# Performance work log

Measured on AMD Instinct MI355X. Metric: run time of the kernel, lower is better.

## Reference

```python
import jax, jax.numpy as jnp
import numpy as np

NODE_FEAT = 200  # F.interpolate size in run_all_node
TOPN = 2         # StitchModel.topn


def _node_feats(img, mask, flow, n_inst, max_pix):
    """Vectorized run_all_node: per-instance gather, linear interp to NODE_FEAT,
    3x3 sign histogram of flow[:2], mean of flow[2]. mask holds labels 1..n_inst;
    max_pix is a static upper bound on pixels per instance."""
    flat = mask.reshape(-1) - 1                       # labels 0..N-1
    order = jnp.argsort(flat)                         # stable sort by label
    counts = jax.ops.segment_sum(jnp.ones_like(flat), flat, num_segments=n_inst)
    starts = jnp.concatenate([jnp.zeros((1,), counts.dtype), jnp.cumsum(counts)[:-1]])
    j = jnp.arange(max_pix)
    pos = starts[:, None] + jnp.minimum(j[None, :], counts[:, None] - 1)
    idx = order[pos]                                  # [N, max_pix] padded pixel indices
    valid = j[None, :] < counts[:, None]              # [N, max_pix]
    iv = img.reshape(-1)[idx]                         # instance intensity profiles
    fx = flow[0].reshape(-1)[idx]
    fy = flow[1].reshape(-1)[idx]
    fz = flow[2].reshape(-1)[idx]
    cf = counts.astype(img.dtype)
    zflow = jnp.where(valid, fz, 0).sum(1) / cf       # flows[-1][m].mean()

    def interp(v, L):                                 # torch linear interp, align_corners=False
        Lf = L.astype(img.dtype)
        p = jnp.clip((jnp.arange(NODE_FEAT, dtype=img.dtype) + 0.5) * (Lf / NODE_FEAT) - 0.5,
                     0.0, Lf - 1.0)
        i0 = jnp.floor(p).astype(jnp.int32)
        i1 = jnp.minimum(i0 + 1, L - 1)
        w = p - i0.astype(img.dtype)
        return v[i0] * (1 - w) + v[i1] * w

    nodes = jax.vmap(interp)(iv, counts)              # [N, 200]
    # hist_flow_vector: bins ordered (x:<0,==0,>0) x (y:<0,==0,>0) -> 3*cx+cy
    cx = jnp.where(fx < 0, 0, jnp.where(fx == 0, 1, 2))
    cy = jnp.where(fy < 0, 0, jnp.where(fy == 0, 1, 2))
    bins = cx * 3 + cy
    oh = (bins[..., None] == jnp.arange(9)) & valid[..., None]
    hist = oh.sum(1).astype(img.dtype)                # [N, 9]
    return jnp.concatenate([nodes, hist], -1), zflow


def setup_inputs() -> dict:
    H = W = 2048
    N = 4096
    pix = (H * W) // N
    key = jax.random.key(0)
    ks = jax.random.split(key, 8)

    def make_mask(k):
        labels = (jnp.arange(H * W, dtype=jnp.int32) // pix) + 1   # labels 1..N
        perm = jax.random.permutation(k, H * W)
        return labels[perm].reshape(H, W)

    def make_bbox(k):
        u = jax.random.uniform(k, (N, 4), jnp.float32)
        centers = u[:, :2] * H
        sizes = u[:, 2:] * 49.0 + 1.0                               # nonzero w/h (asserted)
        return jnp.concatenate([centers, sizes], -1)

    return {
        "img1": jax.random.normal(ks[0], (H, W), jnp.float32),
        "img2": jax.random.normal(ks[1], (H, W), jnp.float32),
        "flow1": jax.random.normal(ks[2], (3, H, W), jnp.float32),
        "flow2": jax.random.normal(ks[3], (3, H, W), jnp.float32),
        "bbox1": make_bbox(ks[4]),
        "bbox2": make_bbox(ks[5]),
        "mask1": make_mask(ks[6]),
        "mask2": make_mask(ks[7]),
    }


def reference(img1, img2, flow1, flow2, bbox1, bbox2, mask1, mask2):
    N1, N2 = bbox1.shape[0], bbox2.shape[0]
    max1 = mask1.size // N1   # static bound on pixels/instance (equal-partition masks)
    max2 = mask2.size // N2
    node1, zf1 = _node_feats(img1, mask1, flow1, N1, max1)
    node2, zf2 = _node_feats(img2, mask2, flow2, N2, max2)
    x = jnp.concatenate([node1, node2], 0)            # [(N1+N2), 209]
    # build_one_graph_low_ram: per row, TOPN smallest center distances
    d = jnp.sqrt(((bbox1[:, None, :2] - bbox2[None, :, :2]) ** 2).sum(-1))  # [N1,N2]
    _, nbr = jax.lax.top_k(-d, TOPN)                  # smallest-first, like argsort[:topn]
    src = jnp.repeat(jnp.arange(N1), TOPN)            # [N1*TOPN]
    dst = nbr.reshape(-1)
    edge_index = jnp.stack([src, dst + N1])           # [2, N1*TOPN]
    edge_attr = jnp.stack([
        zf1[src], zf2[dst],
        bbox1[src, 0] - bbox2[dst, 0],
        bbox1[src, 1] - bbox2[dst, 1],
        bbox1[src, 2] / bbox2[dst, 2],
        bbox1[src, 3] / bbox2[dst, 3],
    ], -1)                                            # [N1*TOPN, 6]
    return x, edge_index, edge_attr
```

## Files before the change

### kernel.cpp

```cpp
#include <hip/hip_runtime.h>
#include <math.h>

#pragma clang fp contract(off)

#define HW      (2048*2048)
#define NI      4096
#define MAXPIX  1024
#define NF      200
#define FEAT    209
#define NE      (NI*2)
#define XSIZE   ((2*NI)*FEAT)
#define EIOFF   XSIZE
#define EAOFF   (EIOFF + 2*NE)

#define S       4096
#define CHK     (HW/S)
#define TOTCHK  (2*CHK)
#define NBPI    256
#define LPB     16
#define NBG     (2*NBPI)
#define REC     (2*HW)
#define CBLK    (TOTCHK/4)
#define BTOT    (LPB*MAXPIX)

template<int NB>
__device__ __forceinline__ unsigned long long match_bits(int v) {
    unsigned long long m = ~0ull;
    #pragma unroll
    for (int bit = 0; bit < NB; ++bit) {
        unsigned long long bb = __ballot((v >> bit) & 1);
        m &= ((v >> bit) & 1) ? bb : ~bb;
    }
    return m;
}

__global__ void __launch_bounds__(256) count_zf_kernel(const int* __restrict__ mask1,
        const int* __restrict__ mask2, const float* __restrict__ flow1,
        const float* __restrict__ flow2, unsigned* __restrict__ cntA,
        float* __restrict__ zfpart) {
    __shared__ unsigned cnt[4][NBPI];
    __shared__ float zfp[NI];
    int w = threadIdx.x >> 6, lane = threadIdx.x & 63;
    for (int j = threadIdx.x; j < 4*NBPI; j += 256) ((unsigned*)cnt)[j] = 0u;
    for (int j = threadIdx.x; j < NI; j += 256) zfp[j] = 0.f;
    __syncthreads();
    int c = blockIdx.x * 4 + w;
    int img = c / CHK;
    const int4*   mask  = (const int4*)(img ? mask2 : mask1);
    const float4* flowz = (const float4*)((img ? flow2 : flow1) + 2L*HW);
    long base4 = (long)(c - img*CHK) * (S/4);
    for (int t = 0; t < S/4; t += 64) {
        int4   l4 = mask[base4 + t + lane];
        float4 fz = flowz[base4 + t + lane];
        atomicAdd(&cnt[w][(l4.x-1) >> 4], 1u);
        atomicAdd(&cnt[w][(l4.y-1) >> 4], 1u);
        atomicAdd(&cnt[w][(l4.z-1) >> 4], 1u);
        atomicAdd(&cnt[w][(l4.w-1) >> 4], 1u);
        atomicAdd(&zfp[l4.x-1], fz.x);
        atomicAdd(&zfp[l4.y-1], fz.y);
        atomicAdd(&zfp[l4.z-1], fz.z);
        atomicAdd(&zfp[l4.w-1], fz.w);
    }
    __syncthreads();
    unsigned* dst = cntA + (long)c * NBPI;
    for (int j = lane; j < NBPI; j += 64) dst[j] = cnt[w][j];
    float* zdst = zfpart + (long)blockIdx.x * NI;
    for (int j = threadIdx.x; j < NI; j += 256) zdst[j] = zfp[j];
}

__global__ void __launch_bounds__(256) scan1_zf_kernel(unsigned* __restrict__ cntA,
        const float* __restrict__ zfpart, float* __restrict__ zfm) {
    __shared__ int wsum[4];
    __shared__ float zsh[4][LPB];
    int gb = blockIdx.x;
    int img = gb >> 8, lb = gb & (NBPI - 1);
    int t = threadIdx.x, lane = t & 63, w = t >> 6;
    const int PER = CHK / 256;
    unsigned e[PER]; int s = 0;
    long base = ((long)img * CHK + (long)t * PER) * NBPI + lb;
    #pragma unroll
    for (int i = 0; i < PER; ++i) { e[i] = cntA[base + (long)i * NBPI]; s += (int)e[i]; }
    int incl = s;
    #pragma unroll
    for (int off = 1; off < 64; off <<= 1) {
        int o = __shfl_up(incl, off);
        if (lane >= off) incl += o;
    }
    if (lane == 63) wsum[w] = incl;
    __syncthreads();
    int add = 0;
    for (int q = 0; q < w; ++q) add += wsum[q];
    unsigned pre = (unsigned)(incl + add - s);
    #pragma unroll
    for (int i = 0; i < PER; ++i) { unsigned cv = e[i]; cntA[base + (long)i * NBPI] = pre; pre += cv; }
    {
        int li0 = gb * LPB;
        int zimg = li0 >> 12, l0 = li0 & (NI-1);
        const float4* zp = (const float4*)(zfpart + (long)zimg*(CBLK/2)*NI + (long)t*NI + l0);
        float4 a0 = zp[0], a1 = zp[1], a2 = zp[2], a3 = zp[3];
        #pragma unroll
        for (int off = 1; off < 64; off <<= 1) {
            a0.x += __shfl_xor(a0.x, off); a0.y += __shfl_xor(a0.y, off);
            a0.z += __shfl_xor(a0.z, off); a0.w += __shfl_xor(a0.w, off);
            a1.x += __shfl_xor(a1.x, off); a1.y += __shfl_xor(a1.y, off);
            a1.z += __shfl_xor(a1.z, off); a1.w += __shfl_xor(a1.w, off);
            a2.x += __shfl_xor(a2.x, off); a2.y += __shfl_xor(a2.y, off);
            a2.z += __shfl_xor(a2.z, off); a2.w += __shfl_xor(a2.w, off);
            a3.x += __shfl_xor(a3.x, off); a3.y += __shfl_xor(a3.y, off);
            a3.z += __shfl_xor(a3.z, off); a3.w += __shfl_xor(a3.w, off);
        }
        if (lane == 0) {
            zsh[w][0]=a0.x; zsh[w][1]=a0.y; zsh[w][2]=a0.z; zsh[w][3]=a0.w;
            zsh[w][4]=a1.x; zsh[w][5]=a1.y; zsh[w][6]=a1.z; zsh[w][7]=a1.w;
            zsh[w][8]=a2.x; zsh[w][9]=a2.y; zsh[w][10]=a2.z; zsh[w][11]=a2.w;
            zsh[w][12]=a3.x; zsh[w][13]=a3.y; zsh[w][14]=a3.z; zsh[w][15]=a3.w;
        }
        __syncthreads();
        if (t < LPB) {
            float sum = zsh[0][t] + zsh[1][t] + zsh[2][t] + zsh[3][t];
            zfm[gb*LPB + t] = sum * (1.0f/(float)MAXPIX);
        }
    }
}

__global__ void __launch_bounds__(512) sort_kernel(
        const float* __restrict__ img1, const float* __restrict__ img2,
        const float* __restrict__ flow1, const float* __restrict__ flow2,
        const int* __restrict__ mask1, const int* __restrict__ mask2,
        const unsigned* __restrict__ cntA,
        float* __restrict__ riv, unsigned char* __restrict__ rmeta) {
    __shared__ float ivs[S];
    __shared__ unsigned short smeta[S];
    __shared__ unsigned short cw[8][NBPI];
    __shared__ int gofs[NBPI];
    __shared__ int wsum[4];
    int t = threadIdx.x, w = t >> 6, lane = t & 63;
    int c = blockIdx.x;
    int img = c / CHK;
    const int*   mask  = img ? mask2  : mask1;
    const float* image = img ? img2   : img1;
    const float* flow  = img ? flow2  : flow1;
    long base = (long)(c - img*CHK) * S;
    for (int j = t; j < 8*NBPI; j += 512) ((unsigned short*)cw)[j] = 0;
    __syncthreads();
    long qbase = base + (long)w * (S/8);
    int   pk[8];
    float piv[8];
    unsigned long long ltmask = (1ull << lane) - 1ull;
    #pragma unroll
    for (int it = 0; it < 8; ++it) {
        long p = qbase + it*64 + lane;
        int l = mask[p] - 1;
        piv[it] = image[p];
        float fx = flow[p], fy = flow[HW + p];
        int cx = fx < 0.f ? 0 : (fx == 0.f ? 1 : 2);
        int cy = fy < 0.f ? 0 : (fy == 0.f ? 1 : 2);
        int bkt = l >> 4;
        unsigned long long m = match_bits<8>(bkt);
        int cb = __popcll(m & ltmask);
        int ct = __popcll(m);
        pk[it] = l | ((cx*3 + cy) << 12) | (cb << 16) | (ct << 22);
        if (cb == 0) cw[w][bkt] += (unsigned short)ct;
    }
    __syncthreads();
    int tot = 0, incl = 0;
    if (t < NBPI) {
        #pragma unroll
        for (int q = 0; q < 8; ++q) tot += cw[q][t];
        incl = tot;
        #pragma unroll
        for (int off = 1; off < 64; off <<= 1) {
            int o = __shfl_up(incl, off);
            if (lane >= off) incl += o;
        }
        if (lane == 63) wsum[w] = incl;
    }
    __syncthreads();
    if (t < NBPI) {
        int add = 0;
        for (int q = 0; q < w; ++q) add += wsum[q];
        int excl = incl + add - tot;
        int run = excl;
        #pragma unroll
        for (int q = 0; q < 8; ++q) {
            int cq = cw[q][t];
            cw[q][t] = (unsigned short)run;
            run += cq;
        }
        gofs[t] = (img*NBPI + t) * BTOT + (int)cntA[(long)c * NBPI + t] - excl;
    }
    __syncthreads();
    #pragma unroll
    for (int it = 0; it < 8; ++it) {
        int pkv = pk[it];
        int l = pkv & 4095, bin = (pkv >> 12) & 15;
        int cb = (pkv >> 16) & 63, ct = (pkv >> 22) & 127;
        int bkt = l >> 4;
        int r0 = (int)cw[w][bkt];
        int dst = r0 + cb;
        if (cb == ct - 1) cw[w][bkt] = (unsigned short)(r0 + ct);
        ivs[dst] = piv[it];
        smeta[dst] = (unsigned short)((bkt << 8) | (bin << 4) | (l & 15));
    }
    __syncthreads();
    for (int j = t; j < S; j += 512) {
        int ms = (int)smeta[j];
        int b = ms >> 8;
        int g = gofs[b] + j;
        riv[g]   = ivs[j];
        rmeta[g] = (unsigned char)(ms & 0xFF);
    }
}

__global__ void __launch_bounds__(512) stageB_kernel(
        const float* __restrict__ riv, const unsigned char* __restrict__ rmeta,
        float* __restrict__ out) {
    __shared__ float acc[LPB * NF];
    __shared__ float s_tw[MAXPIX];
    __shared__ int   s_tk[MAXPIX];
    __shared__ int   hist[LPB * 9];
    __shared__ unsigned qc[8][LPB];
    __shared__ int   cur[8][LPB];
    int t = threadIdx.x, w = t >> 6, lane = t & 63;
    int gb = blockIdx.x;
    for (int j = t; j < LPB*NF; j += 512) acc[j] = 0.f;
    for (int j = t; j < MAXPIX; j += 512) s_tk[j] = -1;
    for (int j = t; j < LPB*9; j += 512) hist[j] = 0;
    for (int j = t; j < 8*LPB; j += 512) ((unsigned*)qc)[j] = 0u;
    __syncthreads();
    if (t < NF) {
        const float Lf = (float)MAXPIX;
        float p = ((float)t + 0.5f) * (Lf / (float)NF) - 0.5f;
        p = fminf(fmaxf(p, 0.0f), Lf - 1.0f);
        int i0 = (int)floorf(p);
        int i1 = min(i0 + 1, MAXPIX - 1);
        float wg = p - (float)i0;
        s_tk[i0] = t; s_tw[i0] = 1.0f - wg;
        s_tk[i1] = t; s_tw[i1] = wg;
    }
    long base = (long)gb * BTOT;
    const int qsz = BTOT / 8;
    int qbeg = w * qsz;
    const int nit = qsz / 64;
    for (int it = 0; it < nit; ++it) {
        int i = qbeg + it*64 + lane;
        atomicAdd(&qc[w][rmeta[base + i] & 15], 1u);
    }
    __syncthreads();
    if (t < LPB) {
        int s = 0;
        #pragma unroll
        for (int q = 0; q < 8; ++q) { cur[q][t] = s; s += (int)qc[q][t]; }
    }
    __syncthreads();
    for (int it = 0; it < nit; ++it) {
        int i = qbeg + it*64 + lane;
        int meta = (int)rmeta[base + i];
        float iv = riv[base + i];
        int ll = meta & 15, bin = meta >> 4;
        unsigned long long m = match_bits<4>(ll);
        int cb = __popcll(m & ((1ull << lane) - 1ull));
        int ct = __popcll(m);
        int r0 = cur[w][ll];
        int rank = r0 + cb;
        if (cb == ct - 1) cur[w][ll] = r0 + ct;
        atomicAdd(&hist[ll*9 + bin], 1);
        int k = s_tk[rank];
        if (k >= 0) atomicAdd(&acc[ll*NF + k], iv * s_tw[rank]);
    }
    __syncthreads();
    if (t < FEAT) {
        for (int r = 0; r < LPB; ++r) {
            long gl = (long)gb * LPB + r;
            out[gl * FEAT + t] = (t < NF) ? acc[r*NF + t] : (float)hist[r*9 + (t - NF)];
        }
    }
}

__device__ __forceinline__ bool better(float d, int j, float d2, int j2) {
    return d < d2 || (d == d2 && j < j2);
}

__global__ void __launch_bounds__(256) edge_kernel(const float* __restrict__ bbox1,
                                                   const float* __restrict__ bbox2,
                                                   const float* __restrict__ zfm,
                                                   float* __restrict__ out) {
    __shared__ float sbx[NI], sby[NI];
    int wave = threadIdx.x >> 6, lane = threadIdx.x & 63;
    for (int r = threadIdx.x; r < NI; r += 256) {
        float4 b = ((const float4*)bbox2)[r];
        sbx[r] = b.x; sby[r] = b.y;
    }
    __syncthreads();
    int i = blockIdx.x * 4 + wave;
    float c1x = bbox1[i*4 + 0], c1y = bbox1[i*4 + 1];
    float d0 = INFINITY; int j0 = 0x7fffffff;
    float d1 = INFINITY; int j1 = 0x7fffffff;
    for (int t = 0; t < NI; t += 64) {
        int j = t + lane;
        float dx = c1x - sbx[j];
        float dy = c1y - sby[j];
        float dsq = dx*dx + dy*dy;
        float d = (float)sqrt((double)dsq);
        if (better(d, j, d0, j0)) { d1 = d0; j1 = j0; d0 = d; j0 = j; }
        else if (better(d, j, d1, j1)) { d1 = d; j1 = j; }
    }
    for (int off = 32; off; off >>= 1) {
        float od0 = __shfl_down(d0, off); int oj0 = __shfl_down(j0, off);
        float od1 = __shfl_down(d1, off); int oj1 = __shfl_down(j1, off);
        if (better(od0, oj0, d0, j0)) {
            if (better(d0, j0, od1, oj1)) { d1 = d0; j1 = j0; }
            else                          { d1 = od1; j1 = oj1; }
            d0 = od0; j0 = oj0;
        } else if (better(od0, oj0, d1, j1)) { d1 = od0; j1 = oj0; }
    }
    if (lane == 0) {
        float z1 = zfm[i];
        int js[2] = { j0, j1 };
        for (int t = 0; t < 2; ++t) {
            int e = i*2 + t, j = js[t];
            out[EIOFF + e]      = (float)i;
            out[EIOFF + NE + e] = (float)(j + NI);
            float* ea = out + EAOFF + (long)e * 6;
            ea[0] = z1;
            ea[1] = zfm[NI + j];
            ea[2] = c1x - bbox2[j*4 + 0];
            ea[3] = c1y - bbox2[j*4 + 1];
            ea[4] = bbox1[i*4 + 2] / bbox2[j*4 + 2];
            ea[5] = bbox1[i*4 + 3] / bbox2[j*4 + 3];
        }
    }
}

extern "C" void kernel_launch(void* const* d_in, const int* in_sizes, int n_in,
                              void* d_out, int out_size, void* d_ws, size_t ws_size,
                              hipStream_t stream) {
    const float* img1  = (const float*)d_in[0];
    const float* img2  = (const float*)d_in[1];
    const float* flow1 = (const float*)d_in[2];
    const float* flow2 = (const float*)d_in[3];
    const float* bbox1 = (const float*)d_in[4];
    const float* bbox2 = (const float*)d_in[5];
    const int*   mask1 = (const int*)d_in[6];
    const int*   mask2 = (const int*)d_in[7];
    float* out = (float*)d_out;

    char* ws = (char*)d_ws;
    size_t off = 0;
    unsigned* cntA   = (unsigned*)(ws + off); off += (size_t)TOTCHK * NBPI * 4;
    float*    riv    = (float*)(ws + off);    off += (size_t)REC * 4;
    float*    zfpart = (float*)(ws + off);    off += (size_t)CBLK * NI * 4;
    float*    zfm    = (float*)(ws + off);    off += 2 * NI * 4;
    unsigned char* rmeta = (unsigned char*)(ws + off); off += (size_t)REC;

    hipLaunchKernelGGL(count_zf_kernel, dim3(CBLK), dim3(256), 0, stream,
                       mask1, mask2, flow1, flow2, cntA, zfpart);
    hipLaunchKernelGGL(scan1_zf_kernel, dim3(NBG), dim3(256), 0, stream,
                       cntA, zfpart, zfm);
    hipLaunchKernelGGL(sort_kernel, dim3(TOTCHK), dim3(512), 0, stream,
                       img1, img2, flow1, flow2, mask1, mask2, cntA, riv, rmeta);
    hipLaunchKernelGGL(stageB_kernel, dim3(NBG), dim3(512), 0, stream,
                       riv, rmeta, out);
    hipLaunchKernelGGL(edge_kernel, dim3(NI/4), dim3(256), 0, stream,
                       bbox1, bbox2, zfm, out);
}
```

Baseline: 312.7 us.

## Double sort chunk size and replace LDS atomics with wave-aggregated counts

Doubles the pixels per sort block so each thread handles 16 pixels, halving the chunk count and the size of the per-chunk count arrays. The zflow partial reduction in scan1 becomes a plain strided sum matching the new partial layout. In stageB, the per-quarter label counting and the histogram updates now use ballot-based match masks with one leader write per group instead of per-lane shared-memory atomics. The metadata bytes are kept packed in registers between the two passes so they are not reloaded. This trades fewer atomics and fewer global reads for more ballots and higher register pressure, and fewer, larger sort blocks.

Result: no change. 311.3 us (-0.4%).

```diff
diff --git a/kernel.cpp b/kernel.cpp
--- a/kernel.cpp
+++ b/kernel.cpp
@@ -13,7 +13,7 @@
 #define EIOFF   XSIZE
 #define EAOFF   (EIOFF + 2*NE)
 
-#define S       4096
+#define S       8192
 #define CHK     (HW/S)
 #define TOTCHK  (2*CHK)
 #define NBPI    256
@@ -71,7 +71,7 @@
 __global__ void __launch_bounds__(256) scan1_zf_kernel(unsigned* __restrict__ cntA,
         const float* __restrict__ zfpart, float* __restrict__ zfm) {
     __shared__ int wsum[4];
-    __shared__ float zsh[4][LPB];
+    __shared__ float zpar[16][LPB];
     int gb = blockIdx.x;
     int img = gb >> 8, lb = gb & (NBPI - 1);
     int t = threadIdx.x, lane = t & 63, w = t >> 6;
@@ -96,30 +96,19 @@
     {
         int li0 = gb * LPB;
         int zimg = li0 >> 12, l0 = li0 & (NI-1);
-        const float4* zp = (const float4*)(zfpart + (long)zimg*(CBLK/2)*NI + (long)t*NI + l0);
-        float4 a0 = zp[0], a1 = zp[1], a2 = zp[2], a3 = zp[3];
-        #pragma unroll
-        for (int off = 1; off < 64; off <<= 1) {
-            a0.x += __shfl_xor(a0.x, off); a0.y += __shfl_xor(a0.y, off);
-            a0.z += __shfl_xor(a0.z, off); a0.w += __shfl_xor(a0.w, off);
-            a1.x += __shfl_xor(a1.x, off); a1.y += __shfl_xor(a1.y, off);
-            a1.z += __shfl_xor(a1.z, off); a1.w += __shfl_xor(a1.w, off);
-            a2.x += __shfl_xor(a2.x, off); a2.y += __shfl_xor(a2.y, off);
-            a2.z += __shfl_xor(a2.z, off); a2.w += __shfl_xor(a2.w, off);
-            a3.x += __shfl_xor(a3.x, off); a3.y += __shfl_xor(a3.y, off);
-            a3.z += __shfl_xor(a3.z, off); a3.w += __shfl_xor(a3.w, off);
-        }
-        if (lane == 0) {
-            zsh[w][0]=a0.x; zsh[w][1]=a0.y; zsh[w][2]=a0.z; zsh[w][3]=a0.w;
-            zsh[w][4]=a1.x; zsh[w][5]=a1.y; zsh[w][6]=a1.z; zsh[w][7]=a1.w;
-            zsh[w][8]=a2.x; zsh[w][9]=a2.y; zsh[w][10]=a2.z; zsh[w][11]=a2.w;
-            zsh[w][12]=a3.x; zsh[w][13]=a3.y; zsh[w][14]=a3.z; zsh[w][15]=a3.w;
-        }
-        __syncthreads();
-        if (t < LPB) {
-            float sum = zsh[0][t] + zsh[1][t] + zsh[2][t] + zsh[3][t];
-            zfm[gb*LPB + t] = sum * (1.0f/(float)MAXPIX);
-        }
+        int lab = t & 15, rg = t >> 4;
+        const float* zp = zfpart + (long)(zimg*(CBLK/2) + rg*8)*NI + l0 + lab;
+        float s8 = 0.f;
+        #pragma unroll
+        for (int k = 0; k < 8; ++k) s8 += zp[(long)k*NI];
+        zpar[rg][lab] = s8;
+    }
+    __syncthreads();
+    if (t < LPB) {
+        float sum = 0.f;
+        #pragma unroll
+        for (int g = 0; g < 16; ++g) sum += zpar[g][t];
+        zfm[gb*LPB + t] = sum * (1.0f/(float)MAXPIX);
     }
 }
 
@@ -133,7 +122,7 @@
     __shared__ unsigned short smeta[S];
     __shared__ unsigned short cw[8][NBPI];
     __shared__ int gofs[NBPI];
-    __shared__ int wsum[4];
+    int* wsum = (int*)smeta;
     int t = threadIdx.x, w = t >> 6, lane = t & 63;
     int c = blockIdx.x;
     int img = c / CHK;
@@ -144,11 +133,11 @@
     for (int j = t; j < 8*NBPI; j += 512) ((unsigned short*)cw)[j] = 0;
     __syncthreads();
     long qbase = base + (long)w * (S/8);
-    int   pk[8];
-    float piv[8];
+    int   pk[16];
+    float piv[16];
     unsigned long long ltmask = (1ull << lane) - 1ull;
     #pragma unroll
-    for (int it = 0; it < 8; ++it) {
+    for (int it = 0; it < 16; ++it) {
         long p = qbase + it*64 + lane;
         int l = mask[p] - 1;
         piv[it] = image[p];
@@ -191,7 +180,7 @@
     }
     __syncthreads();
     #pragma unroll
-    for (int it = 0; it < 8; ++it) {
+    for (int it = 0; it < 16; ++it) {
         int pkv = pk[it];
         int l = pkv & 4095, bin = (pkv >> 12) & 15;
         int cb = (pkv >> 16) & 63, ct = (pkv >> 22) & 127;
@@ -218,15 +207,15 @@
     __shared__ float acc[LPB * NF];
     __shared__ float s_tw[MAXPIX];
     __shared__ int   s_tk[MAXPIX];
-    __shared__ int   hist[LPB * 9];
-    __shared__ unsigned qc[8][LPB];
+    __shared__ int   h8[8][LPB * 9];
+    __shared__ int   qc[8][LPB];
     __shared__ int   cur[8][LPB];
     int t = threadIdx.x, w = t >> 6, lane = t & 63;
     int gb = blockIdx.x;
     for (int j = t; j < LPB*NF; j += 512) acc[j] = 0.f;
     for (int j = t; j < MAXPIX; j += 512) s_tk[j] = -1;
-    for (int j = t; j < LPB*9; j += 512) hist[j] = 0;
-    for (int j = t; j < 8*LPB; j += 512) ((unsigned*)qc)[j] = 0u;
+    for (int j = t; j < 8*LPB*9; j += 512) ((int*)h8)[j] = 0;
+    for (int j = t; j < 8*LPB; j += 512) ((int*)qc)[j] = 0;
     __syncthreads();
     if (t < NF) {
         const float Lf = (float)MAXPIX;
@@ -242,37 +231,65 @@
     const int qsz = BTOT / 8;
     int qbeg = w * qsz;
     const int nit = qsz / 64;
+    unsigned long long ltmask = (1ull << lane) - 1ull;
+    unsigned m4[nit/4];
+    #pragma unroll
+    for (int j = 0; j < nit/4; ++j) m4[j] = 0u;
+    #pragma unroll 4
     for (int it = 0; it < nit; ++it) {
-        int i = qbeg + it*64 + lane;
-        atomicAdd(&qc[w][rmeta[base + i] & 15], 1u);
+        int meta = (int)rmeta[base + qbeg + it*64 + lane];
+        m4[it >> 2] |= (unsigned)meta << (8*(it & 3));
+        unsigned long long m = match_bits<4>(meta & 15);
+        int cb = __popcll(m & ltmask);
+        if (cb == 0) qc[w][meta & 15] += __popcll(m);
     }
     __syncthreads();
     if (t < LPB) {
         int s = 0;
         #pragma unroll
-        for (int q = 0; q < 8; ++q) { cur[q][t] = s; s += (int)qc[q][t]; }
-    }
-    __syncthreads();
+        for (int q = 0; q < 8; ++q) { cur[q][t] = s; s += qc[q][t]; }
+    }
+    __syncthreads();
+    #pragma unroll 4
     for (int it = 0; it < nit; ++it) {
-        int i = qbeg + it*64 + lane;
-        int meta = (int)rmeta[base + i];
-        float iv = riv[base + i];
-        int ll = meta & 15, bin = meta >> 4;
-        unsigned long long m = match_bits<4>(ll);
-        int cb = __popcll(m & ((1ull << lane) - 1ull));
-        int ct = __popcll(m);
+        int meta = (int)(m4[it >> 2] >> (8*(it & 3))) & 255;
+        float iv = riv[base + qbeg + it*64 + lane];
+        int ll = meta & 15;
+        unsigned long long mll = ~0ull, m8;
+        #pragma unroll
+        for (int bit = 0; bit < 4; ++bit) {
+            unsigned long long bb = __ballot((meta >> bit) & 1);
+            mll &= ((meta >> bit) & 1) ? bb : ~bb;
+        }
+        m8 = mll;
+        #pragma unroll
+        for (int bit = 4; bit < 8; ++bit) {
+            unsigned long long bb = __ballot((meta >> bit) & 1);
+            m8 &= ((meta >> bit) & 1) ? bb : ~bb;
+        }
+        int cb = __popcll(mll & ltmask);
+        int ct = __popcll(mll);
         int r0 = cur[w][ll];
         int rank = r0 + cb;
         if (cb == ct - 1) cur[w][ll] = r0 + ct;
-        atomicAdd(&hist[ll*9 + bin], 1);
+        if (__popcll(m8 & ltmask) == 0)
+            h8[w][ll*9 + (meta >> 4)] += __popcll(m8);
         int k = s_tk[rank];
         if (k >= 0) atomicAdd(&acc[ll*NF + k], iv * s_tw[rank]);
     }
     __syncthreads();
     if (t < FEAT) {
         for (int r = 0; r < LPB; ++r) {
+            float v;
+            if (t < NF) v = acc[r*NF + t];
+            else {
+                int hsum = 0;
+                #pragma unroll
+                for (int q = 0; q < 8; ++q) hsum += h8[q][r*9 + (t - NF)];
+                v = (float)hsum;
+            }
             long gl = (long)gb * LPB + r;
-            out[gl * FEAT + t] = (t < NF) ? acc[r*NF + t] : (float)hist[r*9 + (t - NF)];
+            out[gl * FEAT + t] = v;
         }
     }
 }
```
